# Performance work log

Measured on AMD Instinct MI355X. Metric: run time of the kernel, lower is better.

The kernel has to match this reference:

```python
import jax, jax.numpy as jnp
import numpy as np

INF = jnp.float32(np.inf)
LAMBDA_VAL = 1.0
NUM_CLASSES = 10

def setup_inputs() -> dict:
    key = jax.random.key(0)
    k1, k2, k3 = jax.random.split(key, 3)
    N, P, D = 65536, 2048, 64
    x = jax.random.normal(k1, (N, D), dtype=jnp.float32)
    y = jax.random.randint(k2, (N,), 0, NUM_CLASSES)
    prototypes = jax.random.normal(k3, (P, D), dtype=jnp.float32)
    prototype_labels = jnp.arange(P) % NUM_CLASSES
    return {"x": x, "y": y, "prototypes": prototypes, "prototype_labels": prototype_labels}

def _cdist(x, p):
    # Euclidean pairwise distances via the gemm expansion (matches torch.cdist default
    x2 = jnp.sum(x * x, axis=1, keepdims=True)          # [N, 1]
    p2 = jnp.sum(p * p, axis=1)                          # [P]
    sq = x2 + p2[None, :] - 2.0 * (x @ p.T)              # [N, P]
    return jnp.sqrt(jnp.maximum(sq, 0.0))

def reference(x, y, prototypes, prototype_labels):
    distances = _cdist(x, prototypes)                    # [N, P]
    same = prototype_labels[None, :] == y[:, None]       # [N, P] bool
    pos = jnp.min(jnp.where(same, distances, INF), axis=1)   # [N]
    neg = jnp.min(jnp.where(~same, distances, INF), axis=1)  # [N]
    mu = (pos - neg) / (pos + neg)
    loss = jnp.mean(jax.nn.sigmoid(LAMBDA_VAL * mu))
    return loss
```

## Files before the change

### kernel.cpp

```cpp
#include <hip/hip_runtime.h>
#include <math.h>

#define NROWS  65536
#define NPROTO 2048
#define DDIM   64
#define NCLS   10

#define CLS_SLOTS   208
#define CLS_FFRAGS  13
#define CLS_STRIDE  27648
#define CLS_P2_OFF  26624

#define WS_IMG_BYTES   (NCLS * CLS_STRIDE)
#define WS_XA_OFF      WS_IMG_BYTES
#define WS_XA_BYTES    (1024 * 8192)
#define WS_MINS_OFF    (WS_XA_OFF + WS_XA_BYTES)
#define WS_MINS_BYTES  (NCLS * NROWS * 2)
#define WS_X2_OFF      (WS_MINS_OFF + WS_MINS_BYTES)

typedef __attribute__((ext_vector_type(8))) short bf16x8;
typedef __attribute__((ext_vector_type(4))) float f32x4;
typedef __attribute__((ext_vector_type(4))) unsigned int u32x4;

__device__ inline unsigned int f2bf(float f) {
    unsigned int u = __float_as_uint(f);
    return (u + 0x7FFFu + ((u >> 16) & 1u)) >> 16;
}

template <int CTRL>
__device__ inline float rorMin(float v) {
    int t = __builtin_amdgcn_update_dpp(0, __float_as_int(v), CTRL, 0xF, 0xF, false);
    return fminf(v, __int_as_float(t));
}

__global__ __launch_bounds__(256) void prep_kernel(
        const float* __restrict__ x, const float* __restrict__ protos,
        char* __restrict__ wsB, float* __restrict__ out) {
    if (blockIdx.x < 65) {
        int t = blockIdx.x * 256 + threadIdx.x;
        int s = t >> 3, jj = t & 7;
        int L = s / CLS_SLOTS;
        int j = s - L * CLS_SLOTS;
        int cnt = (L < 8) ? 205 : 204;
        bool real = (j < cnt);
        float v[8] = {0.f, 0.f, 0.f, 0.f, 0.f, 0.f, 0.f, 0.f};
        if (real) {
            const float* src = protos + (L + 10 * j) * DDIM + jj * 8;
            float4 a = *(const float4*)src;
            float4 b = *(const float4*)(src + 4);
            v[0] = a.x; v[1] = a.y; v[2] = a.z; v[3] = a.w;
            v[4] = b.x; v[5] = b.y; v[6] = b.z; v[7] = b.w;
        }
        float ss = 0.f;
#pragma unroll
        for (int i = 0; i < 8; i++) ss = fmaf(v[i], v[i], ss);
        ss += __shfl_xor(ss, 1, 64);
        ss += __shfl_xor(ss, 2, 64);
        ss += __shfl_xor(ss, 4, 64);
        unsigned int w[4];
#pragma unroll
        for (int i = 0; i < 4; i++) {
            unsigned int lo = f2bf(-2.f * v[2 * i]);
            unsigned int hi = f2bf(-2.f * v[2 * i + 1]);
            w[i] = lo | (hi << 16);
        }
        size_t base = (size_t)L * CLS_STRIDE;
        *(u32x4*)(wsB + base + (size_t)(j * 8 + (jj ^ (j & 7))) * 16) =
            (u32x4){w[0], w[1], w[2], w[3]};
        if (jj == 0)
            *(float*)(wsB + base + CLS_P2_OFF + j * 4) =
                real ? ss : __builtin_inff();
        if (t == 0) out[0] = 0.f;
    } else {
        int t = (blockIdx.x - 65) * 256 + threadIdx.x;
        int row = t >> 3, j = t & 7;
        const float* src = x + (size_t)row * DDIM + j * 8;
        float4 a = *(const float4*)src;
        float4 b = *(const float4*)(src + 4);
        float v[8] = {a.x, a.y, a.z, a.w, b.x, b.y, b.z, b.w};
        float ss = 0.f;
#pragma unroll
        for (int i = 0; i < 8; i++) ss = fmaf(v[i], v[i], ss);
        ss += __shfl_xor(ss, 1, 64);
        ss += __shfl_xor(ss, 2, 64);
        ss += __shfl_xor(ss, 4, 64);
        unsigned int w[4];
#pragma unroll
        for (int i = 0; i < 4; i++) {
            unsigned int lo = f2bf(v[2 * i]);
            unsigned int hi = f2bf(v[2 * i + 1]);
            w[i] = lo | (hi << 16);
        }
        int rt = row >> 6, m = (row & 63) >> 4, l15 = row & 15;
        int k = j >> 2, q = j & 3;
        size_t off = (size_t)rt * 8192 + m * 2048 + k * 1024 + (q * 16 + l15) * 16;
        *(u32x4*)(wsB + WS_XA_OFF + off) = (u32x4){w[0], w[1], w[2], w[3]};
        if (j == 0) *(float*)(wsB + WS_X2_OFF + (size_t)row * 4) = ss;
    }
}

__global__ __launch_bounds__(512) void glvq_main(
        const char* __restrict__ wsB, _Float16* __restrict__ wsMins) {
    __shared__ __align__(16) char ldsImg[CLS_STRIDE];

    const int tid  = threadIdx.x;
    const int wave = tid >> 6;
    const int lane = tid & 63;
    const int quad = lane >> 4;
    const int l15  = lane & 15;
    const int label = blockIdx.y;
    const float CINF = __builtin_inff();

    const int rowTile = blockIdx.x * 8 + wave;
    const char* xATile = wsB + WS_XA_OFF + (size_t)rowTile * 8192;
    bf16x8 afrag[4][2];
#pragma unroll
    for (int m = 0; m < 4; m++)
#pragma unroll
        for (int k = 0; k < 2; k++)
            afrag[m][k] = *(const bf16x8*)(xATile + m * 2048 + k * 1024 + lane * 16);

    {
        const char* src = wsB + (size_t)label * CLS_STRIDE;
#pragma unroll
        for (int it = 0; it < 3; it++) {
            int ub = it * 512 + wave * 64;
            __builtin_amdgcn_global_load_lds(
                (const __attribute__((address_space(1))) void*)(src + (size_t)ub * 16 + lane * 16),
                (__attribute__((address_space(3))) void*)(ldsImg + (size_t)ub * 16),
                16, 0, 0);
        }
        if (wave < 2) {
            int ub = 1536 + wave * 64;
            __builtin_amdgcn_global_load_lds(
                (const __attribute__((address_space(1))) void*)(src + (size_t)ub * 16 + lane * 16),
                (__attribute__((address_space(3))) void*)(ldsImg + (size_t)ub * 16),
                16, 0, 0);
        }
        if (wave == 2) {
            int ub = 1664;
            __builtin_amdgcn_global_load_lds(
                (const __attribute__((address_space(1))) void*)(src + (size_t)ub * 16 + lane * 16),
                (__attribute__((address_space(3))) void*)(ldsImg + (size_t)ub * 16),
                16, 0, 0);
        }
    }
    asm volatile("s_waitcnt vmcnt(0)" ::: "memory");
    __syncthreads();

    float mMin[4][4];
#pragma unroll
    for (int m = 0; m < 4; m++)
#pragma unroll
        for (int r = 0; r < 4; r++) mMin[m][r] = CINF;

#pragma unroll
    for (int f = 0; f < CLS_FFRAGS; f++) {
        const int s = f * 16 + l15;
        float p2v = *(const float*)(ldsImg + CLS_P2_OFF + s * 4);
        f32x4 p2f = (f32x4){p2v, p2v, p2v, p2v};
        bf16x8 b0 = *(const bf16x8*)(ldsImg + (size_t)(s * 8 + (quad ^ (l15 & 7))) * 16);
        bf16x8 b1 = *(const bf16x8*)(ldsImg + (size_t)(s * 8 + ((4 + quad) ^ (l15 & 7))) * 16);
        f32x4 acc[4];
#pragma unroll
        for (int m = 0; m < 4; m++)
            acc[m] = __builtin_amdgcn_mfma_f32_16x16x32_bf16(
                afrag[m][0], b0, p2f, 0, 0, 0);
#pragma unroll
        for (int m = 0; m < 4; m++)
            acc[m] = __builtin_amdgcn_mfma_f32_16x16x32_bf16(
                afrag[m][1], b1, acc[m], 0, 0, 0);
#pragma unroll
        for (int m = 0; m < 4; m++)
#pragma unroll
            for (int r = 0; r < 4; r++)
                mMin[m][r] = fminf(mMin[m][r], acc[m][r]);
    }

#pragma unroll
    for (int m = 0; m < 4; m++)
#pragma unroll
        for (int r = 0; r < 4; r++) {
            float v = mMin[m][r];
            v = rorMin<0x128>(v);
            v = rorMin<0x124>(v);
            v = rorMin<0x122>(v);
            v = rorMin<0x121>(v);
            mMin[m][r] = v;
        }

    if (l15 == 0) {
        _Float16* plane = wsMins + (size_t)label * NROWS + rowTile * 64;
#pragma unroll
        for (int m = 0; m < 4; m++)
#pragma unroll
            for (int r = 0; r < 4; r++)
                plane[m * 16 + quad * 4 + r] = (_Float16)mMin[m][r];
    }
}

__global__ __launch_bounds__(256) void combine_kernel(
        const int* __restrict__ y, const _Float16* __restrict__ wsMins,
        const float* __restrict__ wsX2, float* __restrict__ out) {
    int row = blockIdx.x * 256 + threadIdx.x;
    int yr = y[row];
    float pos = 0.f, neg = __builtin_inff();
#pragma unroll
    for (int L = 0; L < NCLS; L++) {
        float d = (float)wsMins[(size_t)L * NROWS + row];
        bool isPos = (L == yr);
        pos = isPos ? d : pos;
        neg = isPos ? neg : fminf(neg, d);
    }
    float x2v = wsX2[row];
    float sp = sqrtf(fmaxf(x2v + pos, 0.f));
    float sn = sqrtf(fmaxf(x2v + neg, 0.f));
    float mu = (sp - sn) / (sp + sn);
    float s = 1.f / (1.f + __expf(-mu));

    __shared__ float red[256];
    red[threadIdx.x] = s;
    __syncthreads();
#pragma unroll
    for (int off = 128; off > 0; off >>= 1) {
        if (threadIdx.x < off) red[threadIdx.x] += red[threadIdx.x + off];
        __syncthreads();
    }
    if (threadIdx.x == 0) atomicAdd(out, red[0] * (1.f / (float)NROWS));
}

extern "C" void kernel_launch(void* const* d_in, const int* in_sizes, int n_in,
                              void* d_out, int out_size, void* d_ws, size_t ws_size,
                              hipStream_t stream) {
    const float* x      = (const float*)d_in[0];
    const int*   y      = (const int*)d_in[1];
    const float* protos = (const float*)d_in[2];
    float* out = (float*)d_out;

    char*      wsB    = (char*)d_ws;
    _Float16*  wsMins = (_Float16*)((char*)d_ws + WS_MINS_OFF);
    float*     wsX2   = (float*)((char*)d_ws + WS_X2_OFF);

    prep_kernel<<<65 + NROWS * 8 / 256, 256, 0, stream>>>(x, protos, wsB, out);
    glvq_main<<<dim3(128, 10), 512, 0, stream>>>(wsB, wsMins);
    combine_kernel<<<NROWS / 256, 256, 0, stream>>>(y, wsMins, wsX2, out);
}
```

Baseline: 93.08 us.

## Fuse prep, main, and combine into one cooperative kernel with grid syncs

Result: slower. 160.7 us (+72.6%).

```diff
diff --git a/kernel.cpp b/kernel.cpp
--- a/kernel.cpp
+++ b/kernel.cpp
@@ -1,22 +1,18 @@
 #include <hip/hip_runtime.h>
+#include <hip/hip_cooperative_groups.h>
 #include <math.h>
 
+namespace cg = cooperative_groups;
+
 #define NROWS  65536
-#define NPROTO 2048
 #define DDIM   64
 #define NCLS   10
 
 #define CLS_SLOTS   208
 #define CLS_FFRAGS  13
-#define CLS_STRIDE  27648
+#define CLS_STRIDE  28672
 #define CLS_P2_OFF  26624
-
-#define WS_IMG_BYTES   (NCLS * CLS_STRIDE)
-#define WS_XA_OFF      WS_IMG_BYTES
-#define WS_XA_BYTES    (1024 * 8192)
-#define WS_MINS_OFF    (WS_XA_OFF + WS_XA_BYTES)
-#define WS_MINS_BYTES  (NCLS * NROWS * 2)
-#define WS_X2_OFF      (WS_MINS_OFF + WS_MINS_BYTES)
+#define WS_MINS_OFF (NCLS * CLS_STRIDE)
 
 typedef __attribute__((ext_vector_type(8))) short bf16x8;
 typedef __attribute__((ext_vector_type(4))) float f32x4;
@@ -33,23 +29,37 @@
     return fminf(v, __int_as_float(t));
 }
 
-__global__ __launch_bounds__(256) void prep_kernel(
-        const float* __restrict__ x, const float* __restrict__ protos,
-        char* __restrict__ wsB, float* __restrict__ out) {
-    if (blockIdx.x < 65) {
-        int t = blockIdx.x * 256 + threadIdx.x;
-        int s = t >> 3, jj = t & 7;
-        int L = s / CLS_SLOTS;
-        int j = s - L * CLS_SLOTS;
+__global__ __launch_bounds__(512, 1) void glvq_fused(
+        const float* __restrict__ x, const int* __restrict__ y,
+        const float* __restrict__ protos, char* __restrict__ wsB,
+        _Float16* __restrict__ wsMins, float* __restrict__ out) {
+    __shared__ __align__(16) char ldsImg[2][CLS_STRIDE];
+    __shared__ float sX2[512];
+
+    const int tid  = threadIdx.x;
+    const int wave = tid >> 6;
+    const int lane = tid & 63;
+    const int quad = lane >> 4;
+    const int l15  = lane & 15;
+    const int b    = blockIdx.x;
+    const int slice = b & 127;
+    const int lset  = b >> 7;
+    const float CINF = __builtin_inff();
+
+    int gt = b * 512 + tid;
+    if (gt < 16640) {
+        int s  = gt >> 3, jj = gt & 7;
+        int L  = s / CLS_SLOTS;
+        int j  = s - L * CLS_SLOTS;
         int cnt = (L < 8) ? 205 : 204;
         bool real = (j < cnt);
         float v[8] = {0.f, 0.f, 0.f, 0.f, 0.f, 0.f, 0.f, 0.f};
         if (real) {
             const float* src = protos + (L + 10 * j) * DDIM + jj * 8;
-            float4 a = *(const float4*)src;
-            float4 b = *(const float4*)(src + 4);
-            v[0] = a.x; v[1] = a.y; v[2] = a.z; v[3] = a.w;
-            v[4] = b.x; v[5] = b.y; v[6] = b.z; v[7] = b.w;
+            float4 a  = *(const float4*)src;
+            float4 bb = *(const float4*)(src + 4);
+            v[0] = a.x;  v[1] = a.y;  v[2] = a.z;  v[3] = a.w;
+            v[4] = bb.x; v[5] = bb.y; v[6] = bb.z; v[7] = bb.w;
         }
         float ss = 0.f;
 #pragma unroll
@@ -68,180 +78,159 @@
         *(u32x4*)(wsB + base + (size_t)(j * 8 + (jj ^ (j & 7))) * 16) =
             (u32x4){w[0], w[1], w[2], w[3]};
         if (jj == 0)
-            *(float*)(wsB + base + CLS_P2_OFF + j * 4) =
-                real ? ss : __builtin_inff();
-        if (t == 0) out[0] = 0.f;
-    } else {
-        int t = (blockIdx.x - 65) * 256 + threadIdx.x;
-        int row = t >> 3, j = t & 7;
-        const float* src = x + (size_t)row * DDIM + j * 8;
-        float4 a = *(const float4*)src;
-        float4 b = *(const float4*)(src + 4);
-        float v[8] = {a.x, a.y, a.z, a.w, b.x, b.y, b.z, b.w};
-        float ss = 0.f;
-#pragma unroll
-        for (int i = 0; i < 8; i++) ss = fmaf(v[i], v[i], ss);
-        ss += __shfl_xor(ss, 1, 64);
-        ss += __shfl_xor(ss, 2, 64);
-        ss += __shfl_xor(ss, 4, 64);
-        unsigned int w[4];
+            *(float*)(wsB + base + CLS_P2_OFF + j * 4) = real ? ss : CINF;
+    }
+    if (gt == 0) out[0] = 0.f;
+
+    bf16x8 afrag[4][2];
+#pragma unroll
+    for (int m = 0; m < 4; m++) {
+        const float* xr = x + (size_t)(slice * 512 + wave * 64 + m * 16 + l15) * DDIM;
+        float part = 0.f;
+#pragma unroll
+        for (int k = 0; k < 2; k++) {
+            const float* sp = xr + k * 32 + quad * 8;
+            float4 u0 = *(const float4*)sp;
+            float4 u1 = *(const float4*)(sp + 4);
+            float vv[8] = {u0.x, u0.y, u0.z, u0.w, u1.x, u1.y, u1.z, u1.w};
+            bf16x8 af;
+#pragma unroll
+            for (int i = 0; i < 8; i++) {
+                part = fmaf(vv[i], vv[i], part);
+                af[i] = (short)f2bf(vv[i]);
+            }
+            afrag[m][k] = af;
+        }
+        part += __shfl_xor(part, 16, 64);
+        part += __shfl_xor(part, 32, 64);
+        if (quad == 0) sX2[wave * 64 + m * 16 + l15] = part;
+    }
+
+    __syncthreads();
+    if (wave == 0) __threadfence();
+    cg::this_grid().sync();
+
+    auto stageImg = [&](char* dst, int L) {
+        const char* src = wsB + (size_t)L * CLS_STRIDE;
+        int jb = (wave >= 7) ? 24 : wave * 4;
 #pragma unroll
         for (int i = 0; i < 4; i++) {
-            unsigned int lo = f2bf(v[2 * i]);
-            unsigned int hi = f2bf(v[2 * i + 1]);
-            w[i] = lo | (hi << 16);
-        }
-        int rt = row >> 6, m = (row & 63) >> 4, l15 = row & 15;
-        int k = j >> 2, q = j & 3;
-        size_t off = (size_t)rt * 8192 + m * 2048 + k * 1024 + (q * 16 + l15) * 16;
-        *(u32x4*)(wsB + WS_XA_OFF + off) = (u32x4){w[0], w[1], w[2], w[3]};
-        if (j == 0) *(float*)(wsB + WS_X2_OFF + (size_t)row * 4) = ss;
-    }
-}
-
-__global__ __launch_bounds__(512) void glvq_main(
-        const char* __restrict__ wsB, _Float16* __restrict__ wsMins) {
-    __shared__ __align__(16) char ldsImg[CLS_STRIDE];
-
-    const int tid  = threadIdx.x;
-    const int wave = tid >> 6;
-    const int lane = tid & 63;
-    const int quad = lane >> 4;
-    const int l15  = lane & 15;
-    const int label = blockIdx.y;
-    const float CINF = __builtin_inff();
-
-    const int rowTile = blockIdx.x * 8 + wave;
-    const char* xATile = wsB + WS_XA_OFF + (size_t)rowTile * 8192;
-    bf16x8 afrag[4][2];
-#pragma unroll
-    for (int m = 0; m < 4; m++)
-#pragma unroll
-        for (int k = 0; k < 2; k++)
-            afrag[m][k] = *(const bf16x8*)(xATile + m * 2048 + k * 1024 + lane * 16);
-
-    {
-        const char* src = wsB + (size_t)label * CLS_STRIDE;
-#pragma unroll
-        for (int it = 0; it < 3; it++) {
-            int ub = it * 512 + wave * 64;
+            size_t o = (size_t)(jb + i) * 1024 + (size_t)lane * 16;
             __builtin_amdgcn_global_load_lds(
-                (const __attribute__((address_space(1))) void*)(src + (size_t)ub * 16 + lane * 16),
-                (__attribute__((address_space(3))) void*)(ldsImg + (size_t)ub * 16),
-                16, 0, 0);
-        }
-        if (wave < 2) {
-            int ub = 1536 + wave * 64;
-            __builtin_amdgcn_global_load_lds(
-                (const __attribute__((address_space(1))) void*)(src + (size_t)ub * 16 + lane * 16),
-                (__attribute__((address_space(3))) void*)(ldsImg + (size_t)ub * 16),
-                16, 0, 0);
-        }
-        if (wave == 2) {
-            int ub = 1664;
-            __builtin_amdgcn_global_load_lds(
-                (const __attribute__((address_space(1))) void*)(src + (size_t)ub * 16 + lane * 16),
-                (__attribute__((address_space(3))) void*)(ldsImg + (size_t)ub * 16),
-                16, 0, 0);
-        }
-    }
-    asm volatile("s_waitcnt vmcnt(0)" ::: "memory");
-    __syncthreads();
-
-    float mMin[4][4];
-#pragma unroll
-    for (int m = 0; m < 4; m++)
-#pragma unroll
-        for (int r = 0; r < 4; r++) mMin[m][r] = CINF;
-
-#pragma unroll
-    for (int f = 0; f < CLS_FFRAGS; f++) {
-        const int s = f * 16 + l15;
-        float p2v = *(const float*)(ldsImg + CLS_P2_OFF + s * 4);
-        f32x4 p2f = (f32x4){p2v, p2v, p2v, p2v};
-        bf16x8 b0 = *(const bf16x8*)(ldsImg + (size_t)(s * 8 + (quad ^ (l15 & 7))) * 16);
-        bf16x8 b1 = *(const bf16x8*)(ldsImg + (size_t)(s * 8 + ((4 + quad) ^ (l15 & 7))) * 16);
-        f32x4 acc[4];
+                (const __attribute__((address_space(1))) void*)(src + o),
+                (__attribute__((address_space(3))) void*)(dst + o), 16, 0, 0);
+        }
+    };
+
+    stageImg(ldsImg[0], lset);
+#pragma unroll 1
+    for (int it = 0; it < 5; it++) {
+        const char* cur = ldsImg[it & 1];
+        if (it < 4) {
+            stageImg(ldsImg[(it & 1) ^ 1], lset + 2 * (it + 1));
+            asm volatile("s_waitcnt vmcnt(4)" ::: "memory");
+        } else {
+            asm volatile("s_waitcnt vmcnt(0)" ::: "memory");
+        }
+        __syncthreads();
+
+        float mMin[4][4];
 #pragma unroll
         for (int m = 0; m < 4; m++)
-            acc[m] = __builtin_amdgcn_mfma_f32_16x16x32_bf16(
-                afrag[m][0], b0, p2f, 0, 0, 0);
+#pragma unroll
+            for (int r = 0; r < 4; r++) mMin[m][r] = CINF;
+
+#pragma unroll
+        for (int f = 0; f < CLS_FFRAGS; f++) {
+            const int s = f * 16 + l15;
+            float p2v = *(const float*)(cur + CLS_P2_OFF + s * 4);
+            f32x4 p2f = (f32x4){p2v, p2v, p2v, p2v};
+            bf16x8 b0 = *(const bf16x8*)(cur + (size_t)(s * 8 + (quad ^ (l15 & 7))) * 16);
+            bf16x8 b1 = *(const bf16x8*)(cur + (size_t)(s * 8 + ((4 + quad) ^ (l15 & 7))) * 16);
+            f32x4 acc[4];
+#pragma unroll
+            for (int m = 0; m < 4; m++)
+                acc[m] = __builtin_amdgcn_mfma_f32_16x16x32_bf16(
+                    afrag[m][0], b0, p2f, 0, 0, 0);
+#pragma unroll
+            for (int m = 0; m < 4; m++)
+                acc[m] = __builtin_amdgcn_mfma_f32_16x16x32_bf16(
+                    afrag[m][1], b1, acc[m], 0, 0, 0);
+#pragma unroll
+            for (int m = 0; m < 4; m++)
+#pragma unroll
+                for (int r = 0; r < 4; r++)
+                    mMin[m][r] = fminf(mMin[m][r], acc[m][r]);
+        }
+
 #pragma unroll
         for (int m = 0; m < 4; m++)
-            acc[m] = __builtin_amdgcn_mfma_f32_16x16x32_bf16(
-                afrag[m][1], b1, acc[m], 0, 0, 0);
-#pragma unroll
-        for (int m = 0; m < 4; m++)
-#pragma unroll
-            for (int r = 0; r < 4; r++)
-                mMin[m][r] = fminf(mMin[m][r], acc[m][r]);
-    }
-
-#pragma unroll
-    for (int m = 0; m < 4; m++)
-#pragma unroll
-        for (int r = 0; r < 4; r++) {
-            float v = mMin[m][r];
-            v = rorMin<0x128>(v);
-            v = rorMin<0x124>(v);
-            v = rorMin<0x122>(v);
-            v = rorMin<0x121>(v);
-            mMin[m][r] = v;
-        }
-
-    if (l15 == 0) {
-        _Float16* plane = wsMins + (size_t)label * NROWS + rowTile * 64;
-#pragma unroll
-        for (int m = 0; m < 4; m++)
-#pragma unroll
-            for (int r = 0; r < 4; r++)
-                plane[m * 16 + quad * 4 + r] = (_Float16)mMin[m][r];
-    }
-}
-
-__global__ __launch_bounds__(256) void combine_kernel(
-        const int* __restrict__ y, const _Float16* __restrict__ wsMins,
-        const float* __restrict__ wsX2, float* __restrict__ out) {
-    int row = blockIdx.x * 256 + threadIdx.x;
-    int yr = y[row];
-    float pos = 0.f, neg = __builtin_inff();
-#pragma unroll
-    for (int L = 0; L < NCLS; L++) {
-        float d = (float)wsMins[(size_t)L * NROWS + row];
-        bool isPos = (L == yr);
-        pos = isPos ? d : pos;
-        neg = isPos ? neg : fminf(neg, d);
-    }
-    float x2v = wsX2[row];
-    float sp = sqrtf(fmaxf(x2v + pos, 0.f));
-    float sn = sqrtf(fmaxf(x2v + neg, 0.f));
-    float mu = (sp - sn) / (sp + sn);
-    float s = 1.f / (1.f + __expf(-mu));
-
-    __shared__ float red[256];
-    red[threadIdx.x] = s;
-    __syncthreads();
-#pragma unroll
-    for (int off = 128; off > 0; off >>= 1) {
-        if (threadIdx.x < off) red[threadIdx.x] += red[threadIdx.x + off];
+#pragma unroll
+            for (int r = 0; r < 4; r++) {
+                float v = mMin[m][r];
+                v = rorMin<0x128>(v);
+                v = rorMin<0x124>(v);
+                v = rorMin<0x122>(v);
+                v = rorMin<0x121>(v);
+                mMin[m][r] = v;
+            }
+
+        if (l15 == 0) {
+            _Float16* plane = wsMins + (size_t)(lset + 2 * it) * NROWS
+                              + slice * 512 + wave * 64;
+#pragma unroll
+            for (int m = 0; m < 4; m++)
+#pragma unroll
+                for (int r = 0; r < 4; r++)
+                    plane[m * 16 + quad * 4 + r] = (_Float16)mMin[m][r];
+        }
         __syncthreads();
     }
-    if (threadIdx.x == 0) atomicAdd(out, red[0] * (1.f / (float)NROWS));
+
+    if (wave == 0) __threadfence();
+    cg::this_grid().sync();
+
+    if (b < 128) {
+        int row = b * 512 + tid;
+        int yr = y[row];
+        float pos = 0.f, neg = CINF;
+#pragma unroll
+        for (int L = 0; L < NCLS; L++) {
+            float d = (float)wsMins[(size_t)L * NROWS + row];
+            bool isPos = (L == yr);
+            pos = isPos ? d : pos;
+            neg = isPos ? neg : fminf(neg, d);
+        }
+        float x2v = sX2[tid];
+        float sp = sqrtf(fmaxf(x2v + pos, 0.f));
+        float sn = sqrtf(fmaxf(x2v + neg, 0.f));
+        float mu = (sp - sn) / (sp + sn);
+        float sg = 1.f / (1.f + __expf(-mu));
+
+        float* red = (float*)&ldsImg[0][0];
+        red[tid] = sg;
+        __syncthreads();
+#pragma unroll
+        for (int off = 256; off > 0; off >>= 1) {
+            if (tid < off) red[tid] += red[tid + off];
+            __syncthreads();
+        }
+        if (tid == 0) atomicAdd(out, red[0] * (1.f / (float)NROWS));
+    }
 }
 
 extern "C" void kernel_launch(void* const* d_in, const int* in_sizes, int n_in,
                               void* d_out, int out_size, void* d_ws, size_t ws_size,
                               hipStream_t stream) {
     const float* x      = (const float*)d_in[0];
-    const int*   y      = (const int*)d_in[1];
+    const int*   yk     = (const int*)d_in[1];
     const float* protos = (const float*)d_in[2];
-    float* out = (float*)d_out;
-
+    float*     out    = (float*)d_out;
     char*      wsB    = (char*)d_ws;
     _Float16*  wsMins = (_Float16*)((char*)d_ws + WS_MINS_OFF);
-    float*     wsX2   = (float*)((char*)d_ws + WS_X2_OFF);
-
-    prep_kernel<<<65 + NROWS * 8 / 256, 256, 0, stream>>>(x, protos, wsB, out);
-    glvq_main<<<dim3(128, 10), 512, 0, stream>>>(wsB, wsMins);
-    combine_kernel<<<NROWS / 256, 256, 0, stream>>>(y, wsMins, wsX2, out);
-}
+
+    void* args[] = {(void*)&x, (void*)&yk, (void*)&protos,
+                    (void*)&wsB, (void*)&wsMins, (void*)&out};
+    hipLaunchCooperativeKernel((void*)glvq_fused, dim3(256), dim3(512),
+                               args, 0, stream);
+}
```

## Split each class's prototypes into two halves and shrink blocks to 256 threads

Applied to the files above, without the earlier changes.

Result: slower. 249.7 us (+168.3%).

```diff
diff --git a/kernel.cpp b/kernel.cpp
--- a/kernel.cpp
+++ b/kernel.cpp
@@ -2,21 +2,21 @@
 #include <math.h>
 
 #define NROWS  65536
-#define NPROTO 2048
 #define DDIM   64
 #define NCLS   10
 
-#define CLS_SLOTS   208
-#define CLS_FFRAGS  13
-#define CLS_STRIDE  27648
-#define CLS_P2_OFF  26624
-
-#define WS_IMG_BYTES   (NCLS * CLS_STRIDE)
-#define WS_XA_OFF      WS_IMG_BYTES
-#define WS_XA_BYTES    (1024 * 8192)
-#define WS_MINS_OFF    (WS_XA_OFF + WS_XA_BYTES)
-#define WS_MINS_BYTES  (NCLS * NROWS * 2)
-#define WS_X2_OFF      (WS_MINS_OFF + WS_MINS_BYTES)
+#define HALF_SLOTS  112
+#define HALF_FFRAGS 7
+#define HSTRIDE     16384
+#define HP2_OFF     14336
+#define HCLS        20
+
+#define WS_IMG_BYTES (HCLS * HSTRIDE)
+#define WS_XA_OFF    WS_IMG_BYTES
+#define WS_XA_BYTES  (1024 * 8192)
+#define WS_MINS_OFF  (WS_XA_OFF + WS_XA_BYTES)
+#define WS_MINS_BYTES (HCLS * NROWS * 2)
+#define WS_X2_OFF    (WS_MINS_OFF + WS_MINS_BYTES)
 
 typedef __attribute__((ext_vector_type(8))) short bf16x8;
 typedef __attribute__((ext_vector_type(4))) float f32x4;
@@ -36,16 +36,18 @@
 __global__ __launch_bounds__(256) void prep_kernel(
         const float* __restrict__ x, const float* __restrict__ protos,
         char* __restrict__ wsB, float* __restrict__ out) {
-    if (blockIdx.x < 65) {
-        int t = blockIdx.x * 256 + threadIdx.x;
-        int s = t >> 3, jj = t & 7;
-        int L = s / CLS_SLOTS;
-        int j = s - L * CLS_SLOTS;
+    if (blockIdx.x < 70) {
+        int gt = blockIdx.x * 256 + threadIdx.x;
+        int s = gt >> 3, jj = gt & 7;
+        int h = s / HALF_SLOTS;
+        int jj2 = s - h * HALF_SLOTS;
+        int L = h >> 1;
+        int j = (h & 1) * HALF_SLOTS + jj2;
         int cnt = (L < 8) ? 205 : 204;
         bool real = (j < cnt);
         float v[8] = {0.f, 0.f, 0.f, 0.f, 0.f, 0.f, 0.f, 0.f};
         if (real) {
-            const float* src = protos + (L + 10 * j) * DDIM + jj * 8;
+            const float* src = protos + (size_t)(L + 10 * j) * DDIM + jj * 8;
             float4 a = *(const float4*)src;
             float4 b = *(const float4*)(src + 4);
             v[0] = a.x; v[1] = a.y; v[2] = a.z; v[3] = a.w;
@@ -64,15 +66,15 @@
             unsigned int hi = f2bf(-2.f * v[2 * i + 1]);
             w[i] = lo | (hi << 16);
         }
-        size_t base = (size_t)L * CLS_STRIDE;
-        *(u32x4*)(wsB + base + (size_t)(j * 8 + (jj ^ (j & 7))) * 16) =
+        size_t base = (size_t)h * HSTRIDE;
+        *(u32x4*)(wsB + base + (size_t)(jj2 * 8 + (jj ^ (jj2 & 7))) * 16) =
             (u32x4){w[0], w[1], w[2], w[3]};
         if (jj == 0)
-            *(float*)(wsB + base + CLS_P2_OFF + j * 4) =
+            *(float*)(wsB + base + HP2_OFF + jj2 * 4) =
                 real ? ss : __builtin_inff();
-        if (t == 0) out[0] = 0.f;
+        if (gt == 0) out[0] = 0.f;
     } else {
-        int t = (blockIdx.x - 65) * 256 + threadIdx.x;
+        int t = (blockIdx.x - 70) * 256 + threadIdx.x;
         int row = t >> 3, j = t & 7;
         const float* src = x + (size_t)row * DDIM + j * 8;
         float4 a = *(const float4*)src;
@@ -99,19 +101,31 @@
     }
 }
 
-__global__ __launch_bounds__(512) void glvq_main(
+__global__ __launch_bounds__(256, 8) void glvq_main(
         const char* __restrict__ wsB, _Float16* __restrict__ wsMins) {
-    __shared__ __align__(16) char ldsImg[CLS_STRIDE];
+    __shared__ __align__(16) char ldsImg[HSTRIDE];
 
     const int tid  = threadIdx.x;
     const int wave = tid >> 6;
     const int lane = tid & 63;
     const int quad = lane >> 4;
     const int l15  = lane & 15;
-    const int label = blockIdx.y;
+    const int rx   = blockIdx.x;
+    const int h    = blockIdx.y;
     const float CINF = __builtin_inff();
 
-    const int rowTile = blockIdx.x * 8 + wave;
+    {
+        const char* src = wsB + (size_t)h * HSTRIDE;
+#pragma unroll
+        for (int i = 0; i < 4; i++) {
+            size_t o = (size_t)((wave * 4 + i) * 64 + lane) * 16;
+            __builtin_amdgcn_global_load_lds(
+                (const __attribute__((address_space(1))) void*)(src + o),
+                (__attribute__((address_space(3))) void*)(ldsImg + o), 16, 0, 0);
+        }
+    }
+
+    const int rowTile = rx * 4 + wave;
     const char* xATile = wsB + WS_XA_OFF + (size_t)rowTile * 8192;
     bf16x8 afrag[4][2];
 #pragma unroll
@@ -120,31 +134,6 @@
         for (int k = 0; k < 2; k++)
             afrag[m][k] = *(const bf16x8*)(xATile + m * 2048 + k * 1024 + lane * 16);
 
-    {
-        const char* src = wsB + (size_t)label * CLS_STRIDE;
-#pragma unroll
-        for (int it = 0; it < 3; it++) {
-            int ub = it * 512 + wave * 64;
-            __builtin_amdgcn_global_load_lds(
-                (const __attribute__((address_space(1))) void*)(src + (size_t)ub * 16 + lane * 16),
-                (__attribute__((address_space(3))) void*)(ldsImg + (size_t)ub * 16),
-                16, 0, 0);
-        }
-        if (wave < 2) {
-            int ub = 1536 + wave * 64;
-            __builtin_amdgcn_global_load_lds(
-                (const __attribute__((address_space(1))) void*)(src + (size_t)ub * 16 + lane * 16),
-                (__attribute__((address_space(3))) void*)(ldsImg + (size_t)ub * 16),
-                16, 0, 0);
-        }
-        if (wave == 2) {
-            int ub = 1664;
-            __builtin_amdgcn_global_load_lds(
-                (const __attribute__((address_space(1))) void*)(src + (size_t)ub * 16 + lane * 16),
-                (__attribute__((address_space(3))) void*)(ldsImg + (size_t)ub * 16),
-                16, 0, 0);
-        }
-    }
     asm volatile("s_waitcnt vmcnt(0)" ::: "memory");
     __syncthreads();
 
@@ -155,12 +144,12 @@
         for (int r = 0; r < 4; r++) mMin[m][r] = CINF;
 
 #pragma unroll
-    for (int f = 0; f < CLS_FFRAGS; f++) {
+    for (int f = 0; f < HALF_FFRAGS; f++) {
         const int s = f * 16 + l15;
-        float p2v = *(const float*)(ldsImg + CLS_P2_OFF + s * 4);
+        float p2v = *(const float*)(ldsImg + HP2_OFF + s * 4);
         f32x4 p2f = (f32x4){p2v, p2v, p2v, p2v};
-        bf16x8 b0 = *(const bf16x8*)(ldsImg + (size_t)(s * 8 + (quad ^ (l15 & 7))) * 16);
-        bf16x8 b1 = *(const bf16x8*)(ldsImg + (size_t)(s * 8 + ((4 + quad) ^ (l15 & 7))) * 16);
+        bf16x8 b0 = *(const bf16x8*)(ldsImg + (size_t)(s * 8 + (quad ^ (s & 7))) * 16);
+        bf16x8 b1 = *(const bf16x8*)(ldsImg + (size_t)(s * 8 + ((4 + quad) ^ (s & 7))) * 16);
         f32x4 acc[4];
 #pragma unroll
         for (int m = 0; m < 4; m++)
@@ -190,7 +179,7 @@
         }
 
     if (l15 == 0) {
-        _Float16* plane = wsMins + (size_t)label * NROWS + rowTile * 64;
+        _Float16* plane = wsMins + (size_t)h * NROWS + rowTile * 64;
 #pragma unroll
         for (int m = 0; m < 4; m++)
 #pragma unroll
@@ -200,16 +189,18 @@
 }
 
 __global__ __launch_bounds__(256) void combine_kernel(
-        const int* __restrict__ y, const _Float16* __restrict__ wsMins,
-        const float* __restrict__ wsX2, float* __restrict__ out) {
+        const int* __restrict__ y, const char* __restrict__ wsB,
+        float* __restrict__ out) {
+    const _Float16* wsMins = (const _Float16*)(wsB + WS_MINS_OFF);
+    const float*    wsX2   = (const float*)(wsB + WS_X2_OFF);
     int row = blockIdx.x * 256 + threadIdx.x;
     int yr = y[row];
-    float pos = 0.f, neg = __builtin_inff();
-#pragma unroll
-    for (int L = 0; L < NCLS; L++) {
-        float d = (float)wsMins[(size_t)L * NROWS + row];
-        bool isPos = (L == yr);
-        pos = isPos ? d : pos;
+    float pos = __builtin_inff(), neg = __builtin_inff();
+#pragma unroll
+    for (int hc = 0; hc < HCLS; hc++) {
+        float d = (float)wsMins[(size_t)hc * NROWS + row];
+        bool isPos = ((hc >> 1) == yr);
+        pos = isPos ? fminf(pos, d) : pos;
         neg = isPos ? neg : fminf(neg, d);
     }
     float x2v = wsX2[row];
@@ -233,15 +224,13 @@
                               void* d_out, int out_size, void* d_ws, size_t ws_size,
                               hipStream_t stream) {
     const float* x      = (const float*)d_in[0];
-    const int*   y      = (const int*)d_in[1];
+    const int*   yk     = (const int*)d_in[1];
     const float* protos = (const float*)d_in[2];
     float* out = (float*)d_out;
-
-    char*      wsB    = (char*)d_ws;
-    _Float16*  wsMins = (_Float16*)((char*)d_ws + WS_MINS_OFF);
-    float*     wsX2   = (float*)((char*)d_ws + WS_X2_OFF);
-
-    prep_kernel<<<65 + NROWS * 8 / 256, 256, 0, stream>>>(x, protos, wsB, out);
-    glvq_main<<<dim3(128, 10), 512, 0, stream>>>(wsB, wsMins);
-    combine_kernel<<<NROWS / 256, 256, 0, stream>>>(y, wsMins, wsX2, out);
-}
+    char*  wsB = (char*)d_ws;
+    _Float16* wsMins = (_Float16*)(wsB + WS_MINS_OFF);
+
+    prep_kernel<<<70 + NROWS * 8 / 256, 256, 0, stream>>>(x, protos, wsB, out);
+    glvq_main<<<dim3(256, HCLS), 256, 0, stream>>>(wsB, wsMins);
+    combine_kernel<<<NROWS / 256, 256, 0, stream>>>(yk, wsB, out);
+}
```
